# Optimization experiments

Hardware: AMD Instinct MI355X
Metric: run time of the kernel (lower is better)

Reference implementation:

```python
import jax, jax.numpy as jnp
import numpy as np

N_POINTS = 2_000_000
GRID = 256  # voxel grid resolution (D=H=W), production-scale stand-in for source's 128


def setup_inputs() -> dict:
    key = jax.random.key(0)
    k1, k2, k3 = jax.random.split(key, 3)
    coords = jax.random.uniform(k1, (N_POINTS, 3), dtype=jnp.float32,
                                minval=-0.95, maxval=0.95)
    registration_pred = jax.random.normal(k2, (N_POINTS, 3), dtype=jnp.float32) * 0.02
    registration_gt = jax.random.normal(k3, (N_POINTS, 3), dtype=jnp.float32) * 0.02
    return {"registration_pred": registration_pred,
            "registration_gt": registration_gt,
            "coords": coords}


def _splat(pts, size):
    """Trilinear scatter (adjoint of F.grid_sample, align_corners=False,
    zero padding). pts: [N,3] normalized coords in (x,y,z) order mapping to
    (W,H,D). Splats weight 1 per point. Returns [D,H,W] volume."""
    D = H = W = size
    # grid_sample align_corners=False unnormalization: p = ((g+1)*size - 1)/2
    x = ((pts[:, 0] + 1.0) * W - 1.0) * 0.5
    y = ((pts[:, 1] + 1.0) * H - 1.0) * 0.5
    z = ((pts[:, 2] + 1.0) * D - 1.0) * 0.5
    x0f, y0f, z0f = jnp.floor(x), jnp.floor(y), jnp.floor(z)
    fx, fy, fz = x - x0f, y - y0f, z - z0f  # fractional offsets
    x0, y0, z0 = x0f.astype(jnp.int32), y0f.astype(jnp.int32), z0f.astype(jnp.int32)
    vol = jnp.zeros(D * H * W, dtype=pts.dtype)
    for dz in (0, 1):
        wz = fz if dz else (1.0 - fz)
        for dy in (0, 1):
            wy = fy if dy else (1.0 - fy)
            for dx in (0, 1):
                wx = fx if dx else (1.0 - fx)
                xi, yi, zi = x0 + dx, y0 + dy, z0 + dz
                valid = ((xi >= 0) & (xi < W) & (yi >= 0) & (yi < H)
                         & (zi >= 0) & (zi < D))
                w = jnp.where(valid, wx * wy * wz, 0.0)
                idx = jnp.where(valid, (zi * H + yi) * W + xi, 0)
                vol = vol.at[idx].add(w)
    return vol.reshape(D, H, W)


def reference(registration_pred, registration_gt, coords):
    pred_vol = _splat(coords + registration_pred, GRID)
    gt_vol = _splat(coords + registration_gt, GRID)
    # HuberLoss(reduction='sum', delta=1.0)
    d = pred_vol - gt_vol
    ad = jnp.abs(d)
    return jnp.sum(jnp.where(ad <= 1.0, 0.5 * d * d, ad - 0.5))
```

## Files before the change

kernel.cpp:

```cpp
#include <hip/hip_runtime.h>

#define GRID_RES 256
#define NCELLS 1024
#define NB 1024
#define BCAP 6144
#define NPT 2

#define W_SCALE 2097152.0f
#define INV_W (1.0f / 2097152.0f)
#define L_SCALE 512.0f
#define INV_L (1.0f / 512.0f)

struct CEv { unsigned w0, w1q, xyz; };

__device__ __forceinline__ CEv make_cev(float px, float py, float pz,
                                        unsigned sign) {
    float x = ((px + 1.0f) * (float)GRID_RES - 1.0f) * 0.5f;
    float y = ((py + 1.0f) * (float)GRID_RES - 1.0f) * 0.5f;
    float z = ((pz + 1.0f) * (float)GRID_RES - 1.0f) * 0.5f;
    float xf = floorf(x), yf = floorf(y), zf = floorf(z);
    int x0 = (int)xf, y0 = (int)yf, z0 = (int)zf;
    unsigned qx = (unsigned)((x - xf) * 65535.0f + 0.5f);
    unsigned qy = (unsigned)((y - yf) * 65535.0f + 0.5f);
    unsigned qz = (unsigned)((z - zf) * 16383.0f + 0.5f);
    bool valid = (x0 >= -1) & (x0 <= 255) & (y0 >= -1) & (y0 <= 255) &
                 (z0 >= -1) & (z0 <= 255);
    CEv e;
    e.w0 = qx | (qy << 16);
    e.w1q = qz | (sign << 31);
    e.xyz = valid ? ((unsigned)(x0 + 1) | ((unsigned)(y0 + 1) << 10) |
                     ((unsigned)(z0 + 1) << 20) | (1u << 30))
                  : 0u;
    return e;
}

template <typename F>
__device__ __forceinline__ void enum_cells(const CEv& e, F&& emit) {
    if (!(e.xyz & (1u << 30))) return;
    int x0 = (int)(e.xyz & 1023u) - 1;
    int y0 = (int)((e.xyz >> 10) & 1023u) - 1;
    int z0 = (int)((e.xyz >> 20) & 1023u) - 1;
    int cxs[2], cys[2], czs[2];
    int nx = 0, ny = 0, nz = 0;
    {
        bool vA = (x0 >= 0) & (x0 <= 255);
        bool vB = (x0 >= -1) & (x0 <= 254);
        int cA = x0 >> 5, cB = (x0 + 1) >> 5;
        if (vA) cxs[nx++] = cA;
        if (vB && (!vA || cB != cA)) cxs[nx++] = cB;
    }
    {
        bool vA = (y0 >= 0) & (y0 <= 255);
        bool vB = (y0 >= -1) & (y0 <= 254);
        int cA = y0 >> 5, cB = (y0 + 1) >> 5;
        if (vA) cys[ny++] = cA;
        if (vB && (!vA || cB != cA)) cys[ny++] = cB;
    }
    {
        bool vA = (z0 >= 0) & (z0 <= 255);
        bool vB = (z0 >= -1) & (z0 <= 254);
        int cA = z0 >> 4, cB = (z0 + 1) >> 4;
        if (vA) czs[nz++] = cA;
        if (vB && (!vA || cB != cA)) czs[nz++] = cB;
    }
    for (int a = 0; a < nz; ++a) {
        int cz = czs[a];
        unsigned lz = (unsigned)(z0 - (cz << 4) + 1);
        for (int b = 0; b < ny; ++b) {
            int cy = cys[b];
            unsigned ly = (unsigned)(y0 - (cy << 5) + 1);
            for (int c = 0; c < nx; ++c) {
                int cx = cxs[c];
                unsigned lx = (unsigned)(x0 - (cx << 5) + 1);
                int cell = (cz << 6) | (cy << 3) | cx;
                unsigned w1 = e.w1q | (lx << 14) | (ly << 20) | (lz << 26);
                emit(cell, e.w0, w1);
            }
        }
    }
}

__global__ __launch_bounds__(1024) void bin_kernel(
    const float* __restrict__ pred, const float* __restrict__ gt,
    const float* __restrict__ coords, unsigned* __restrict__ segOff,
    unsigned* __restrict__ segCnt, uint2* __restrict__ payload,
    int* __restrict__ lossAcc, int n) {
    __shared__ unsigned h[NCELLS];
    __shared__ unsigned wtot[16];
    int b = blockIdx.x;
    int t = threadIdx.x;
    if (b == 0 && t == 0) lossAcc[0] = 0;
    h[t] = 0;
    __syncthreads();

    int chunk = (n + NB - 1) / NB;
    int start = b * chunk;
    int end = min(start + chunk, n);
    const float3* c3 = (const float3*)coords;
    const float3* p3 = (const float3*)pred;
    const float3* g3 = (const float3*)gt;

    CEv ev[2 * NPT];
#pragma unroll
    for (int k = 0; k < NPT; ++k) {
        int i = start + t + (k << 10);
        if (i < end) {
            float3 c = c3[i];
            float3 p = p3[i];
            float3 g = g3[i];
            ev[2 * k] = make_cev(c.x + p.x, c.y + p.y, c.z + p.z, 0u);
            ev[2 * k + 1] = make_cev(c.x + g.x, c.y + g.y, c.z + g.z, 1u);
        } else {
            ev[2 * k].xyz = 0;
            ev[2 * k + 1].xyz = 0;
        }
    }

#pragma unroll
    for (int k = 0; k < 2 * NPT; ++k)
        enum_cells(ev[k], [&](int cell, unsigned, unsigned) {
            atomicAdd(&h[cell], 1u);
        });
    __syncthreads();

    unsigned x = h[t];
    unsigned incl = x;
    int lane = t & 63, wid = t >> 6;
#pragma unroll
    for (int off = 1; off < 64; off <<= 1) {
        unsigned y = __shfl_up(incl, off, 64);
        if (lane >= off) incl += y;
    }
    if (lane == 63) wtot[wid] = incl;
    __syncthreads();
    if (t == 0) {
        unsigned r = 0;
#pragma unroll
        for (int w = 0; w < 16; ++w) { unsigned v = wtot[w]; wtot[w] = r; r += v; }
    }
    __syncthreads();
    unsigned offE = incl - x + wtot[wid];
    segOff[(size_t)b * NCELLS + t] = offE;
    segCnt[(size_t)b * NCELLS + t] = x;
    __syncthreads();
    h[t] = offE;
    __syncthreads();

    uint2* pb = payload + (size_t)b * BCAP;
#pragma unroll
    for (int k = 0; k < 2 * NPT; ++k)
        enum_cells(ev[k], [&](int cell, unsigned w0, unsigned w1) {
            unsigned slot = atomicAdd(&h[cell], 1u);
            if (slot < (unsigned)BCAP) pb[slot] = make_uint2(w0, w1);
        });
}

__global__ __launch_bounds__(1024) void accum_kernel(
    const uint2* __restrict__ payload, const unsigned* __restrict__ segOff,
    const unsigned* __restrict__ segCnt, int* __restrict__ lossAcc) {
    __shared__ int v[16384];
    __shared__ unsigned sbase[NB + 1];
    __shared__ unsigned pbase[NB];
    __shared__ unsigned w16[16];
    __shared__ float wsum[16];
    int c = blockIdx.x;
    int t = threadIdx.x;
#pragma unroll
    for (int j = 0; j < 16; ++j) v[t + (j << 10)] = 0;

    int lane = t & 63, wid = t >> 6;
    unsigned cnt = segCnt[(size_t)t * NCELLS + c];
    unsigned off = segOff[(size_t)t * NCELLS + c];
    unsigned incl = cnt;
#pragma unroll
    for (int o = 1; o < 64; o <<= 1) {
        unsigned y = __shfl_up(incl, o, 64);
        if (lane >= o) incl += y;
    }
    if (lane == 63) w16[wid] = incl;
    __syncthreads();
    if (t == 0) {
        unsigned r = 0;
#pragma unroll
        for (int w = 0; w < 16; ++w) { unsigned q = w16[w]; w16[w] = r; r += q; }
        sbase[NB] = r;
    }
    __syncthreads();
    if (t == 0) sbase[NB] = w16[15] + incl - cnt + cnt;
    __syncthreads();
    sbase[t] = incl - cnt + w16[wid];
    pbase[t] = (unsigned)t * (unsigned)BCAP + off;
    if (t == 1023) sbase[NB] = incl + w16[wid];
    __syncthreads();

    unsigned total = sbase[NB];
    for (unsigned i = t; i < total; i += 1024) {
        int lo = 0, hi = NB - 1;
#pragma unroll
        for (int s = 0; s < 10; ++s) {
            int mid = (lo + hi + 1) >> 1;
            if (sbase[mid] <= i) lo = mid; else hi = mid - 1;
        }
        uint2 p = payload[(size_t)pbase[lo] + (i - sbase[lo])];
        float fx = (float)(p.x & 0xFFFFu) * (1.0f / 65535.0f);
        float fy = (float)(p.x >> 16) * (1.0f / 65535.0f);
        float fz = (float)(p.y & 0x3FFFu) * (1.0f / 16383.0f);
        int lx = (int)((p.y >> 14) & 63u);
        int ly = (int)((p.y >> 20) & 63u);
        int lz = (int)((p.y >> 26) & 31u);
        float s = (p.y >> 31) ? -W_SCALE : W_SCALE;
        float wxs[2] = {1.0f - fx, fx};
        float wys[2] = {1.0f - fy, fy};
        float wzs[2] = {1.0f - fz, fz};
        int xb = lx - 1, yb = ly - 1, zb = lz - 1;
#pragma unroll
        for (int dz = 0; dz < 2; ++dz) {
            int rz = zb + dz;
            if ((unsigned)rz > 15u) continue;
            float wz = s * wzs[dz];
#pragma unroll
            for (int dy = 0; dy < 2; ++dy) {
                int ry = yb + dy;
                if ((unsigned)ry > 31u) continue;
                float wyz = wz * wys[dy];
#pragma unroll
                for (int dx = 0; dx < 2; ++dx) {
                    int rx = xb + dx;
                    if ((unsigned)rx > 31u) continue;
                    int iw = __float2int_rn(wyz * wxs[dx]);
                    atomicAdd(&v[(rz << 10) | (ry << 5) | rx], iw);
                }
            }
        }
    }
    __syncthreads();

    float acc = 0.0f;
#pragma unroll
    for (int j = 0; j < 16; ++j) {
        int val = v[t + (j << 10)];
        float d = (float)val * INV_W;
        float ad = fabsf(d);
        acc += (ad <= 1.0f) ? 0.5f * d * d : ad - 0.5f;
    }
#pragma unroll
    for (int o = 32; o > 0; o >>= 1) acc += __shfl_down(acc, o, 64);
    if (lane == 0) wsum[wid] = acc;
    __syncthreads();
    if (t == 0) {
        float tsum = 0.0f;
#pragma unroll
        for (int w = 0; w < 16; ++w) tsum += wsum[w];
        atomicAdd(lossAcc, __float2int_rn(tsum * L_SCALE));
    }
}

__global__ void finalize_kernel(const int* __restrict__ lossAcc,
                                float* __restrict__ out) {
    out[0] = (float)lossAcc[0] * INV_L;
}

extern "C" void kernel_launch(void* const* d_in, const int* in_sizes, int n_in,
                              void* d_out, int out_size, void* d_ws, size_t ws_size,
                              hipStream_t stream) {
    const float* reg_pred = (const float*)d_in[0];
    const float* reg_gt   = (const float*)d_in[1];
    const float* coords   = (const float*)d_in[2];
    float* out = (float*)d_out;

    char* ws = (char*)d_ws;
    int* lossAcc = (int*)ws;
    unsigned* segOff = (unsigned*)(ws + 256);
    unsigned* segCnt = segOff + (size_t)NB * NCELLS;
    uint2* payload = (uint2*)((char*)segCnt + (size_t)NB * NCELLS * 4);

    int n = in_sizes[0] / 3;

    bin_kernel<<<NB, 1024, 0, stream>>>(reg_pred, reg_gt, coords, segOff,
                                        segCnt, payload, lossAcc, n);
    accum_kernel<<<NCELLS, 1024, 0, stream>>>(payload, segOff, segCnt,
                                              lossAcc);
    finalize_kernel<<<1, 1, 0, stream>>>(lossAcc, out);
}
```

Baseline: 167.2 us.

## Stage binned events in LDS, pack offset/count, fuse finalize into accum

The bin kernel now enumerates each point's cell events once and stages them (cell id and payload words) in shared memory, then scatters them from there instead of recomputing the events in a second pass. Per-block segment offset and count are packed into a single 32-bit word, halving that table's traffic. The finalize kernel is removed: the last accum block, found through an atomic counter, writes the output. The staging buffer uses about 40KB of LDS and silently drops events beyond SCAP, and the 16-bit packing assumes per-block counts stay below 65536.

New measurement: 183.3 us. 9.6% more time.

```diff
diff --git a/kernel.cpp b/kernel.cpp
--- a/kernel.cpp
+++ b/kernel.cpp
@@ -4,6 +4,7 @@
 #define NCELLS 1024
 #define NB 1024
 #define BCAP 6144
+#define SCAP 4864
 #define NPT 2
 
 #define W_SCALE 2097152.0f
@@ -11,10 +12,9 @@
 #define L_SCALE 512.0f
 #define INV_L (1.0f / 512.0f)
 
-struct CEv { unsigned w0, w1q, xyz; };
-
-__device__ __forceinline__ CEv make_cev(float px, float py, float pz,
-                                        unsigned sign) {
+template <typename F>
+__device__ __forceinline__ void enum_event(float px, float py, float pz,
+                                           unsigned sign, F&& emit) {
     float x = ((px + 1.0f) * (float)GRID_RES - 1.0f) * 0.5f;
     float y = ((py + 1.0f) * (float)GRID_RES - 1.0f) * 0.5f;
     float z = ((pz + 1.0f) * (float)GRID_RES - 1.0f) * 0.5f;
@@ -23,23 +23,9 @@
     unsigned qx = (unsigned)((x - xf) * 65535.0f + 0.5f);
     unsigned qy = (unsigned)((y - yf) * 65535.0f + 0.5f);
     unsigned qz = (unsigned)((z - zf) * 16383.0f + 0.5f);
-    bool valid = (x0 >= -1) & (x0 <= 255) & (y0 >= -1) & (y0 <= 255) &
-                 (z0 >= -1) & (z0 <= 255);
-    CEv e;
-    e.w0 = qx | (qy << 16);
-    e.w1q = qz | (sign << 31);
-    e.xyz = valid ? ((unsigned)(x0 + 1) | ((unsigned)(y0 + 1) << 10) |
-                     ((unsigned)(z0 + 1) << 20) | (1u << 30))
-                  : 0u;
-    return e;
-}
-
-template <typename F>
-__device__ __forceinline__ void enum_cells(const CEv& e, F&& emit) {
-    if (!(e.xyz & (1u << 30))) return;
-    int x0 = (int)(e.xyz & 1023u) - 1;
-    int y0 = (int)((e.xyz >> 10) & 1023u) - 1;
-    int z0 = (int)((e.xyz >> 20) & 1023u) - 1;
+    unsigned w0 = qx | (qy << 16);
+    unsigned w1q = qz | (sign << 31);
+
     int cxs[2], cys[2], czs[2];
     int nx = 0, ny = 0, nz = 0;
     {
@@ -73,8 +59,8 @@
                 int cx = cxs[c];
                 unsigned lx = (unsigned)(x0 - (cx << 5) + 1);
                 int cell = (cz << 6) | (cy << 3) | cx;
-                unsigned w1 = e.w1q | (lx << 14) | (ly << 20) | (lz << 26);
-                emit(cell, e.w0, w1);
+                unsigned w1 = w1q | (lx << 14) | (ly << 20) | (lz << 26);
+                emit(cell, w0, w1);
             }
         }
     }
@@ -82,15 +68,19 @@
 
 __global__ __launch_bounds__(1024) void bin_kernel(
     const float* __restrict__ pred, const float* __restrict__ gt,
-    const float* __restrict__ coords, unsigned* __restrict__ segOff,
-    unsigned* __restrict__ segCnt, uint2* __restrict__ payload,
-    int* __restrict__ lossAcc, int n) {
+    const float* __restrict__ coords, unsigned* __restrict__ pkT,
+    uint2* __restrict__ payload, int* __restrict__ lossAcc, int n) {
+    __shared__ unsigned short sC[SCAP];
+    __shared__ unsigned sW0[SCAP];
+    __shared__ unsigned sW1[SCAP];
     __shared__ unsigned h[NCELLS];
     __shared__ unsigned wtot[16];
+    __shared__ unsigned scnt;
     int b = blockIdx.x;
     int t = threadIdx.x;
-    if (b == 0 && t == 0) lossAcc[0] = 0;
+    if (b == 0 && t == 0) { lossAcc[0] = 0; lossAcc[1] = 0; }
     h[t] = 0;
+    if (t == 0) scnt = 0;
     __syncthreads();
 
     int chunk = (n + NB - 1) / NB;
@@ -100,7 +90,15 @@
     const float3* p3 = (const float3*)pred;
     const float3* g3 = (const float3*)gt;
 
-    CEv ev[2 * NPT];
+    auto stage = [&](int cell, unsigned w0, unsigned w1) {
+        unsigned slot = atomicAdd(&scnt, 1u);
+        if (slot < (unsigned)SCAP) {
+            sC[slot] = (unsigned short)cell;
+            sW0[slot] = w0;
+            sW1[slot] = w1;
+            atomicAdd(&h[cell], 1u);
+        }
+    };
 #pragma unroll
     for (int k = 0; k < NPT; ++k) {
         int i = start + t + (k << 10);
@@ -108,19 +106,10 @@
             float3 c = c3[i];
             float3 p = p3[i];
             float3 g = g3[i];
-            ev[2 * k] = make_cev(c.x + p.x, c.y + p.y, c.z + p.z, 0u);
-            ev[2 * k + 1] = make_cev(c.x + g.x, c.y + g.y, c.z + g.z, 1u);
-        } else {
-            ev[2 * k].xyz = 0;
-            ev[2 * k + 1].xyz = 0;
-        }
-    }
-
-#pragma unroll
-    for (int k = 0; k < 2 * NPT; ++k)
-        enum_cells(ev[k], [&](int cell, unsigned, unsigned) {
-            atomicAdd(&h[cell], 1u);
-        });
+            enum_event(c.x + p.x, c.y + p.y, c.z + p.z, 0u, stage);
+            enum_event(c.x + g.x, c.y + g.y, c.z + g.z, 1u, stage);
+        }
+    }
     __syncthreads();
 
     unsigned x = h[t];
@@ -140,24 +129,23 @@
     }
     __syncthreads();
     unsigned offE = incl - x + wtot[wid];
-    segOff[(size_t)b * NCELLS + t] = offE;
-    segCnt[(size_t)b * NCELLS + t] = x;
+    pkT[(size_t)b * NCELLS + t] = offE | (x << 16);
     __syncthreads();
     h[t] = offE;
     __syncthreads();
 
     uint2* pb = payload + (size_t)b * BCAP;
-#pragma unroll
-    for (int k = 0; k < 2 * NPT; ++k)
-        enum_cells(ev[k], [&](int cell, unsigned w0, unsigned w1) {
-            unsigned slot = atomicAdd(&h[cell], 1u);
-            if (slot < (unsigned)BCAP) pb[slot] = make_uint2(w0, w1);
-        });
+    unsigned m = min(scnt, (unsigned)SCAP);
+    for (unsigned j = t; j < m; j += 1024) {
+        int cell = (int)sC[j];
+        unsigned slot = atomicAdd(&h[cell], 1u);
+        pb[slot] = make_uint2(sW0[j], sW1[j]);
+    }
 }
 
 __global__ __launch_bounds__(1024) void accum_kernel(
-    const uint2* __restrict__ payload, const unsigned* __restrict__ segOff,
-    const unsigned* __restrict__ segCnt, int* __restrict__ lossAcc) {
+    const uint2* __restrict__ payload, const unsigned* __restrict__ pkT,
+    int* __restrict__ lossAcc, float* __restrict__ out) {
     __shared__ int v[16384];
     __shared__ unsigned sbase[NB + 1];
     __shared__ unsigned pbase[NB];
@@ -169,8 +157,9 @@
     for (int j = 0; j < 16; ++j) v[t + (j << 10)] = 0;
 
     int lane = t & 63, wid = t >> 6;
-    unsigned cnt = segCnt[(size_t)t * NCELLS + c];
-    unsigned off = segOff[(size_t)t * NCELLS + c];
+    unsigned pk = pkT[(size_t)t * NCELLS + c];
+    unsigned off = pk & 0xFFFFu;
+    unsigned cnt = pk >> 16;
     unsigned incl = cnt;
 #pragma unroll
     for (int o = 1; o < 64; o <<= 1) {
@@ -183,14 +172,12 @@
         unsigned r = 0;
 #pragma unroll
         for (int w = 0; w < 16; ++w) { unsigned q = w16[w]; w16[w] = r; r += q; }
-        sbase[NB] = r;
-    }
-    __syncthreads();
-    if (t == 0) sbase[NB] = w16[15] + incl - cnt + cnt;
-    __syncthreads();
-    sbase[t] = incl - cnt + w16[wid];
+    }
+    __syncthreads();
+    unsigned sb = incl - cnt + w16[wid];
+    sbase[t] = sb;
     pbase[t] = (unsigned)t * (unsigned)BCAP + off;
-    if (t == 1023) sbase[NB] = incl + w16[wid];
+    if (t == 1023) sbase[NB] = sb + cnt;
     __syncthreads();
 
     unsigned total = sbase[NB];
@@ -251,13 +238,15 @@
         float tsum = 0.0f;
 #pragma unroll
         for (int w = 0; w < 16; ++w) tsum += wsum[w];
-        atomicAdd(lossAcc, __float2int_rn(tsum * L_SCALE));
-    }
-}
-
-__global__ void finalize_kernel(const int* __restrict__ lossAcc,
-                                float* __restrict__ out) {
-    out[0] = (float)lossAcc[0] * INV_L;
+        atomicAdd(&lossAcc[0], __float2int_rn(tsum * L_SCALE));
+        __threadfence();
+        unsigned old = atomicAdd((unsigned*)&lossAcc[1], 1u);
+        if (old == (unsigned)(NCELLS - 1)) {
+            __threadfence();
+            int fin = atomicAdd(&lossAcc[0], 0);
+            out[0] = (float)fin * INV_L;
+        }
+    }
 }
 
 extern "C" void kernel_launch(void* const* d_in, const int* in_sizes, int n_in,
@@ -270,15 +259,12 @@
 
     char* ws = (char*)d_ws;
     int* lossAcc = (int*)ws;
-    unsigned* segOff = (unsigned*)(ws + 256);
-    unsigned* segCnt = segOff + (size_t)NB * NCELLS;
-    uint2* payload = (uint2*)((char*)segCnt + (size_t)NB * NCELLS * 4);
+    unsigned* pkT = (unsigned*)(ws + 256);
+    uint2* payload = (uint2*)((char*)pkT + (size_t)NB * NCELLS * 4);
 
     int n = in_sizes[0] / 3;
 
-    bin_kernel<<<NB, 1024, 0, stream>>>(reg_pred, reg_gt, coords, segOff,
-                                        segCnt, payload, lossAcc, n);
-    accum_kernel<<<NCELLS, 1024, 0, stream>>>(payload, segOff, segCnt,
-                                              lossAcc);
-    finalize_kernel<<<1, 1, 0, stream>>>(lossAcc, out);
-}
+    bin_kernel<<<NB, 1024, 0, stream>>>(reg_pred, reg_gt, coords, pkT,
+                                        payload, lossAcc, n);
+    accum_kernel<<<NCELLS, 1024, 0, stream>>>(payload, pkT, lossAcc, out);
+}
```
